# Kernel optimization log

Measured on AMD Instinct MI355X. Metric: run time of the kernel, lower is better.

## Reference

```python
import jax, jax.numpy as jnp
import numpy as np

B, N, D, K = 16, 512, 256, 12  # batch, nodes, node_dim, num edge types (4 arg + 4 arg' + punct +/- + no_edges +/-)
ITERATION_STEPS = 1


def setup_inputs() -> dict:
    key = jax.random.key(0)
    ks = jax.random.split(key, 8)
    node = jax.random.normal(ks[0], (B, N, D), dtype=jnp.float32)
    node_mask = jax.random.randint(ks[1], (B, N), 0, 2, dtype=jnp.int32)
    graphs = jax.random.randint(ks[2], (K, B, N, N), 0, 2, dtype=jnp.int32)
    s = 1.0 / np.sqrt(D)
    Ww = jax.random.normal(ks[3], (1, D), dtype=jnp.float32) * s   # _node_weight_fc
    bw = jnp.zeros((1,), dtype=jnp.float32)
    Ws = jax.random.normal(ks[4], (D, D), dtype=jnp.float32) * s   # _self_node_fc
    bs = jnp.zeros((D,), dtype=jnp.float32)
    Wk = jax.random.normal(ks[5], (K, D, D), dtype=jnp.float32) * s  # 12 bias-free per-edge-type linears
    return {"node": node, "Ww": Ww, "bw": bw, "Ws": Ws, "bs": bs, "Wk": Wk,
            "node_mask": node_mask, "graphs": graphs}


def reference(node, Ww, bw, Ws, bs, Wk, node_mask, graphs):
    dt = node.dtype
    mask = node_mask.astype(dt)
    eye = jnp.eye(N, dtype=dt)
    # dd_graph = mask_row * mask_col * (1 - diag)
    dd = mask[:, None, :] * mask[:, :, None] * (1.0 - eye)          # [B,N,N]
    g = dd[None] * graphs.astype(dt)                                # [K,B,N,N] masked adjacencies
    neigh = g.sum(axis=(0, 3))                                      # [B,N] total neighbor count
    neigh = jnp.where(neigh >= 1, neigh, jnp.ones((), dt))

    all_w = []
    for _ in range(ITERATION_STEPS):
        # (1) node relatedness
        w = jax.nn.sigmoid(node @ Ww.T + bw)[..., 0]                # [B,N]
        all_w.append(w)
        self_info = node @ Ws.T + bs                                # [B,N,D]
        # (2) message propagation for all 12 edge types, batched
        trans = jnp.einsum('bnd,ked->kbne', node, Wk)               # [K,B,N,D] per-type linear (x @ W.T)
        wg = w[None, :, None, :] * g                                # [K,B,N,N] masked node weights
        agg = jnp.einsum('kbmn,kbnd->bmd', wg, trans) / neigh[..., None]
        # (3) update
        node = jax.nn.relu(self_info + agg)

    all_weight = jnp.stack(all_w, axis=1)                           # [B,steps,N]
    return node, all_weight
```

## Files before the change

kernel.cpp:

```cpp
#include <hip/hip_runtime.h>
#include <hip/hip_bf16.h>
#include <math.h>

#define BB 16
#define NN 512
#define DD 256
#define KK 12

typedef __bf16 bf16x8 __attribute__((ext_vector_type(8)));
typedef __bf16 bf16x4 __attribute__((ext_vector_type(4)));
typedef float  f32x4  __attribute__((ext_vector_type(4)));

#define WS_WM     0
#define WS_NCNT   32768
#define WS_MASKBF 65536
#define WS_NODEBF 81920
#define WS_NODET  4276224
#define WS_WKBF   8470528
#define WS_WSBF   10043392
#define WS_AGG    10174464

__global__ __launch_bounds__(256) void k1_prep(const float* __restrict__ node,
        const float* __restrict__ Ww, const float* __restrict__ bw,
        const int* __restrict__ node_mask,
        float* __restrict__ wm, __bf16* __restrict__ maskbf,
        __bf16* __restrict__ node_bf, float* __restrict__ all_w) {
    int t = threadIdx.x;
    int lane = t & 63;
    int row = blockIdx.x * 4 + (t >> 6);
    const float4 nv = *(const float4*)(node + (size_t)row * DD + lane * 4);
    const float4 wv = *(const float4*)(Ww + lane * 4);
    float dot = nv.x*wv.x + nv.y*wv.y + nv.z*wv.z + nv.w*wv.w;
    #pragma unroll
    for (int off = 32; off > 0; off >>= 1) dot += __shfl_xor(dot, off);
    float w = 1.0f / (1.0f + expf(-(dot + bw[0])));
    int mk = node_mask[row];
    if (lane == 0) {
        wm[row]     = w * (float)mk;
        all_w[row]  = w;
        maskbf[row] = (__bf16)(float)mk;
    }
    bf16x4 nb = {(__bf16)nv.x, (__bf16)nv.y, (__bf16)nv.z, (__bf16)nv.w};
    *(bf16x4*)(node_bf + (size_t)row * DD + lane * 4) = nb;
}

__global__ __launch_bounds__(256) void k1b_convert(const float* __restrict__ Wk,
        const float* __restrict__ Ws, __bf16* __restrict__ Wk_bf, __bf16* __restrict__ Ws_bf) {
    const int KDD = KK * DD * DD;
    int idx = (blockIdx.x * 256 + threadIdx.x) * 4;
    if (idx < KDD) {
        float4 v = *(const float4*)(Wk + idx);
        bf16x4 o = {(__bf16)v.x, (__bf16)v.y, (__bf16)v.z, (__bf16)v.w};
        *(bf16x4*)(Wk_bf + idx) = o;
    } else {
        int j = idx - KDD;
        if (j < DD * DD) {
            float4 v = *(const float4*)(Ws + j);
            bf16x4 o = {(__bf16)v.x, (__bf16)v.y, (__bf16)v.z, (__bf16)v.w};
            *(bf16x4*)(Ws_bf + j) = o;
        }
    }
}

__global__ __launch_bounds__(256) void k2_transpose(const float* __restrict__ node,
        const float* __restrict__ wm, __bf16* __restrict__ dst) {
    __shared__ float tile[64][65];
    int bx = blockIdx.x;
    int b = bx >> 5; int rest = bx & 31; int nt = rest >> 2; int dt = rest & 3;
    int n0 = nt * 64, d0 = dt * 64;
    int t = threadIdx.x;
    #pragma unroll
    for (int i = 0; i < 16; i++) {
        int idx = i * 256 + t;
        int n = idx >> 6, d = idx & 63;
        tile[n][d] = node[((size_t)(b * NN + n0 + n)) * DD + d0 + d];
    }
    __syncthreads();
    #pragma unroll
    for (int i = 0; i < 16; i++) {
        int idx = i * 256 + t;
        int d = idx >> 6, n = idx & 63;
        float w = wm[b * NN + n0 + n];
        dst[((size_t)(b * DD + d0 + d)) * NN + n0 + n] = (__bf16)(tile[n][d] * w);
    }
}

__global__ __launch_bounds__(512, 2) void k45_partial(const int* __restrict__ graphs,
        const __bf16* __restrict__ maskbf, const __bf16* __restrict__ node_t,
        const __bf16* __restrict__ Wk_bf, float* __restrict__ Agg, int* __restrict__ ncnt) {
    __shared__ __align__(16) __bf16 Abf[32][520];
    __shared__ __align__(16) __bf16 Tk[32][264];
    __shared__ float cntp[8][32];
    int bx = blockIdx.x;
    int b  = (bx & 7) + 8 * ((bx >> 3) & 1);
    int kh = (bx >> 4) & 1;
    int mt = bx >> 5;
    int m0 = mt * 32;
    int t = threadIdx.x;
    int lane = t & 63;
    int w = t >> 6;
    int q = lane >> 4;
    int l16 = lane & 15;
    int esub = w * 32;
    int dsub = w * 32;

    int crow = t >> 7;
    int ccol = (t & 127) * 4;

    f32x4 accO[2][2];
    #pragma unroll
    for (int i = 0; i < 2; i++)
        #pragma unroll
        for (int j = 0; j < 2; j++) accO[i][j] = (f32x4){0.f, 0.f, 0.f, 0.f};
    f32x4 accC[2];
    accC[0] = (f32x4){0.f, 0.f, 0.f, 0.f};
    accC[1] = (f32x4){0.f, 0.f, 0.f, 0.f};

    int4 g[8];
    {
        const int4* gb = (const int4*)(graphs + ((size_t)((kh * 6 * BB + b) * NN + m0)) * NN);
        #pragma unroll
        for (int u = 0; u < 8; u++) g[u] = gb[u * 512 + t];
    }

    #pragma unroll 1
    for (int kc = 0; kc < 6; kc++) {
        int k = kh * 6 + kc;
        #pragma unroll
        for (int u = 0; u < 8; u++) {
            int row = u * 4 + crow;
            unsigned p0 = (unsigned)g[u].x | ((unsigned)g[u].y << 16);
            unsigned p1 = (unsigned)g[u].z | ((unsigned)g[u].w << 16);
            unsigned drel = (unsigned)(m0 + row - ccol);
            if (drel < 2u)      p0 &= ~(0xFFFFu << (16 * drel));
            else if (drel < 4u) p1 &= ~(0xFFFFu << (16 * (drel - 2)));
            uint2 st; st.x = p0 * 0x3F80u; st.y = p1 * 0x3F80u;
            *(uint2*)&Abf[row][ccol] = st;
        }
        __syncthreads();

        if (kc < 5) {
            const int4* gb = (const int4*)(graphs + ((size_t)(((k + 1) * BB + b) * NN + m0)) * NN);
            #pragma unroll
            for (int u = 0; u < 8; u++) g[u] = gb[u * 512 + t];
        }

        f32x4 accT[2][2];
        #pragma unroll
        for (int i = 0; i < 2; i++)
            #pragma unroll
            for (int j = 0; j < 2; j++) accT[i][j] = (f32x4){0.f, 0.f, 0.f, 0.f};
        #pragma unroll
        for (int kk = 0; kk < 16; kk++) {
            int n0c = kk * 32;
            bf16x8 af[2], bfr[2];
            #pragma unroll
            for (int fm = 0; fm < 2; fm++)
                af[fm] = *(const bf16x8*)&Abf[fm * 16 + l16][n0c + q * 8];
            #pragma unroll
            for (int fd = 0; fd < 2; fd++)
                bfr[fd] = *(const bf16x8*)(node_t +
                    ((size_t)(b * DD + esub + fd * 16 + l16)) * NN + n0c + q * 8);
            #pragma unroll
            for (int fm = 0; fm < 2; fm++)
                #pragma unroll
                for (int fd = 0; fd < 2; fd++)
                    accT[fm][fd] = __builtin_amdgcn_mfma_f32_16x16x32_bf16(
                        af[fm], bfr[fd], accT[fm][fd], 0, 0, 0);
            if ((kk >> 1) == w) {
                bf16x8 bfm = (bf16x8){0,0,0,0,0,0,0,0};
                if (l16 == 0)
                    bfm = *(const bf16x8*)(maskbf + b * NN + n0c + q * 8);
                accC[0] = __builtin_amdgcn_mfma_f32_16x16x32_bf16(af[0], bfm, accC[0], 0, 0, 0);
                accC[1] = __builtin_amdgcn_mfma_f32_16x16x32_bf16(af[1], bfm, accC[1], 0, 0, 0);
            }
        }
        #pragma unroll
        for (int fm = 0; fm < 2; fm++)
            #pragma unroll
            for (int fd = 0; fd < 2; fd++) {
                int col = esub + fd * 16 + l16;
                #pragma unroll
                for (int r = 0; r < 4; r++)
                    Tk[fm * 16 + q * 4 + r][col] = (__bf16)accT[fm][fd][r];
            }
        __syncthreads();

        #pragma unroll
        for (int ee = 0; ee < 8; ee++) {
            int e0c = ee * 32;
            bf16x8 afT[2], bw2[2];
            #pragma unroll
            for (int fm = 0; fm < 2; fm++)
                afT[fm] = *(const bf16x8*)&Tk[fm * 16 + l16][e0c + q * 8];
            #pragma unroll
            for (int fd = 0; fd < 2; fd++)
                bw2[fd] = *(const bf16x8*)(Wk_bf +
                    ((size_t)(k * DD + dsub + fd * 16 + l16)) * DD + e0c + q * 8);
            #pragma unroll
            for (int fm = 0; fm < 2; fm++)
                #pragma unroll
                for (int fd = 0; fd < 2; fd++)
                    accO[fm][fd] = __builtin_amdgcn_mfma_f32_16x16x32_bf16(
                        afT[fm], bw2[fd], accO[fm][fd], 0, 0, 0);
        }
    }

    if (l16 == 0) {
        #pragma unroll
        for (int fm = 0; fm < 2; fm++)
            #pragma unroll
            for (int r = 0; r < 4; r++)
                cntp[w][fm * 16 + q * 4 + r] = accC[fm][r];
    }
    __syncthreads();
    if (t < 32) {
        float c = 0.0f;
        #pragma unroll
        for (int w8 = 0; w8 < 8; w8++) c += cntp[w8][t];
        atomicAdd(&ncnt[b * NN + m0 + t], (int)(c + 0.5f));
    }

    float* Ah = Agg + (size_t)kh * BB * NN * DD;
    #pragma unroll
    for (int fm = 0; fm < 2; fm++)
        #pragma unroll
        for (int fd = 0; fd < 2; fd++) {
            int d = dsub + fd * 16 + l16;
            #pragma unroll
            for (int r = 0; r < 4; r++) {
                int m = m0 + fm * 16 + q * 4 + r;
                Ah[((size_t)(b * NN + m)) * DD + d] = accO[fm][fd][r];
            }
        }
}

__global__ __launch_bounds__(256) void k6_epilogue(const float* __restrict__ Agg,
        const __bf16* __restrict__ node_bf, const __bf16* __restrict__ Ws_bf,
        const float* __restrict__ bs, const int* __restrict__ ncnt,
        const int* __restrict__ node_mask, float* __restrict__ out) {
    __shared__ float sm[16];
    int bx = blockIdx.x;
    int b = bx & 15;
    int mt = bx >> 4;
    int m0 = mt * 16;
    int t = threadIdx.x;
    int lane = t & 63;
    int w = t >> 6;
    int q = lane >> 4;
    int l16 = lane & 15;
    int dsub = w * 64;

    if (t < 16) {
        int c = ncnt[b * NN + m0 + t];
        int mk = node_mask[b * NN + m0 + t];
        sm[t] = (float)mk / (float)(c >= 1 ? c : 1);
    }

    f32x4 accS[4];
    #pragma unroll
    for (int i = 0; i < 4; i++) accS[i] = (f32x4){0.f, 0.f, 0.f, 0.f};
    #pragma unroll
    for (int ee = 0; ee < 8; ee++) {
        int e0c = ee * 32;
        bf16x8 afS = *(const bf16x8*)(node_bf +
            ((size_t)(b * NN + m0 + l16)) * DD + e0c + q * 8);
        bf16x8 bwS[4];
        #pragma unroll
        for (int fd = 0; fd < 4; fd++)
            bwS[fd] = *(const bf16x8*)(Ws_bf +
                ((size_t)(dsub + fd * 16 + l16)) * DD + e0c + q * 8);
        #pragma unroll
        for (int fd = 0; fd < 4; fd++)
            accS[fd] = __builtin_amdgcn_mfma_f32_16x16x32_bf16(afS, bwS[fd], accS[fd], 0, 0, 0);
    }
    __syncthreads();

    const float* A0 = Agg;
    const float* A1 = Agg + (size_t)BB * NN * DD;
    #pragma unroll
    for (int fd = 0; fd < 4; fd++) {
        int d = dsub + fd * 16 + l16;
        float bsv = bs[d];
        #pragma unroll
        for (int r = 0; r < 4; r++) {
            int m = m0 + q * 4 + r;
            size_t idx = ((size_t)(b * NN + m)) * DD + d;
            float v = sm[q * 4 + r] * (A0[idx] + A1[idx]) + accS[fd][r] + bsv;
            out[idx] = fmaxf(v, 0.0f);
        }
    }
}

extern "C" void kernel_launch(void* const* d_in, const int* in_sizes, int n_in,
                              void* d_out, int out_size, void* d_ws, size_t ws_size,
                              hipStream_t stream) {
    const float* node      = (const float*)d_in[0];
    const float* Ww        = (const float*)d_in[1];
    const float* bw        = (const float*)d_in[2];
    const float* Ws        = (const float*)d_in[3];
    const float* bs        = (const float*)d_in[4];
    const float* Wk        = (const float*)d_in[5];
    const int*   node_mask = (const int*)d_in[6];
    const int*   graphs    = (const int*)d_in[7];
    float* out   = (float*)d_out;
    float* all_w = out + (size_t)BB * NN * DD;

    char* ws = (char*)d_ws;
    float*  wm      = (float*)(ws + WS_WM);
    int*    ncnt    = (int*)(ws + WS_NCNT);
    __bf16* maskbf  = (__bf16*)(ws + WS_MASKBF);
    __bf16* node_bf = (__bf16*)(ws + WS_NODEBF);
    __bf16* node_t  = (__bf16*)(ws + WS_NODET);
    __bf16* Wk_bf   = (__bf16*)(ws + WS_WKBF);
    __bf16* Ws_bf   = (__bf16*)(ws + WS_WSBF);
    float*  Agg     = (float*)(ws + WS_AGG);

    hipMemsetAsync(ncnt, 0, BB * NN * sizeof(int), stream);
    k1_prep    <<<2048, 256, 0, stream>>>(node, Ww, bw, node_mask, wm, maskbf, node_bf, all_w);
    k1b_convert<<< 832, 256, 0, stream>>>(Wk, Ws, Wk_bf, Ws_bf);
    k2_transpose<<<512, 256, 0, stream>>>(node, wm, node_t);
    k45_partial<<< 512, 512, 0, stream>>>(graphs, maskbf, node_t, Wk_bf, Agg, ncnt);
    k6_epilogue<<< 512, 256, 0, stream>>>(Agg, node_bf, Ws_bf, bs, ncnt, node_mask, out);
}
```

Measured before the change: 373.6 us.

## Split edge types four ways with smaller blocks and blob-layout partial aggregates

The main aggregation kernel now splits the 12 edge types into four groups of three instead of two groups of six. It launches 1024 blocks of 256 threads, and each wave covers 64 output columns instead of 32. Graph loads are no longer prefetched across iterations; they are loaded directly per half-tile. Partial aggregates are written as contiguous per-thread float4 blobs, and the epilogue reads and sums the four partials with vector loads over 32-row tiles. The aim is more parallelism and coalesced partial stores, at the cost of twice the partial-aggregate traffic and lost load/compute overlap.

```diff
diff --git a/kernel.cpp b/kernel.cpp
--- a/kernel.cpp
+++ b/kernel.cpp
@@ -19,6 +19,7 @@
 #define WS_WKBF   8470528
 #define WS_WSBF   10043392
 #define WS_AGG    10174464
+#define AGG_KQ_STRIDE 2097152
 
 __global__ __launch_bounds__(256) void k1_prep(const float* __restrict__ node,
         const float* __restrict__ Ww, const float* __restrict__ bw,
@@ -85,89 +86,83 @@
     }
 }
 
-__global__ __launch_bounds__(512, 2) void k45_partial(const int* __restrict__ graphs,
+__global__ __launch_bounds__(256) void k45_partial(const int* __restrict__ graphs,
         const __bf16* __restrict__ maskbf, const __bf16* __restrict__ node_t,
-        const __bf16* __restrict__ Wk_bf, float* __restrict__ Agg, int* __restrict__ ncnt) {
+        const __bf16* __restrict__ Wk_bf, float* __restrict__ AggBlob, int* __restrict__ ncnt) {
     __shared__ __align__(16) __bf16 Abf[32][520];
     __shared__ __align__(16) __bf16 Tk[32][264];
-    __shared__ float cntp[8][32];
+    __shared__ float cntp[4][32];
     int bx = blockIdx.x;
     int b  = (bx & 7) + 8 * ((bx >> 3) & 1);
-    int kh = (bx >> 4) & 1;
-    int mt = bx >> 5;
+    int kq = (bx >> 4) & 3;
+    int mt = bx >> 6;
     int m0 = mt * 32;
     int t = threadIdx.x;
     int lane = t & 63;
     int w = t >> 6;
     int q = lane >> 4;
     int l16 = lane & 15;
-    int esub = w * 32;
-    int dsub = w * 32;
-
-    int crow = t >> 7;
-    int ccol = (t & 127) * 4;
-
-    f32x4 accO[2][2];
+    int esub = w * 64;
+    int dsub = w * 64;
+
+    int rowpar = t >> 7;
+    int ccol   = (t & 127) * 4;
+
+    f32x4 accO[2][4];
     #pragma unroll
     for (int i = 0; i < 2; i++)
         #pragma unroll
-        for (int j = 0; j < 2; j++) accO[i][j] = (f32x4){0.f, 0.f, 0.f, 0.f};
+        for (int j = 0; j < 4; j++) accO[i][j] = (f32x4){0.f, 0.f, 0.f, 0.f};
     f32x4 accC[2];
     accC[0] = (f32x4){0.f, 0.f, 0.f, 0.f};
     accC[1] = (f32x4){0.f, 0.f, 0.f, 0.f};
 
-    int4 g[8];
-    {
-        const int4* gb = (const int4*)(graphs + ((size_t)((kh * 6 * BB + b) * NN + m0)) * NN);
-        #pragma unroll
-        for (int u = 0; u < 8; u++) g[u] = gb[u * 512 + t];
-    }
-
     #pragma unroll 1
-    for (int kc = 0; kc < 6; kc++) {
-        int k = kh * 6 + kc;
-        #pragma unroll
-        for (int u = 0; u < 8; u++) {
-            int row = u * 4 + crow;
-            unsigned p0 = (unsigned)g[u].x | ((unsigned)g[u].y << 16);
-            unsigned p1 = (unsigned)g[u].z | ((unsigned)g[u].w << 16);
-            unsigned drel = (unsigned)(m0 + row - ccol);
-            if (drel < 2u)      p0 &= ~(0xFFFFu << (16 * drel));
-            else if (drel < 4u) p1 &= ~(0xFFFFu << (16 * (drel - 2)));
-            uint2 st; st.x = p0 * 0x3F80u; st.y = p1 * 0x3F80u;
-            *(uint2*)&Abf[row][ccol] = st;
+    for (int kc = 0; kc < 3; kc++) {
+        int k = kq * 3 + kc;
+        #pragma unroll
+        for (int h = 0; h < 2; h++) {
+            const int4* gb = (const int4*)(graphs + ((size_t)((k * BB + b) * NN + m0 + h * 16)) * NN);
+            int4 g[8];
+            #pragma unroll
+            for (int u = 0; u < 8; u++) g[u] = gb[u * 256 + t];
+            #pragma unroll
+            for (int u = 0; u < 8; u++) {
+                int row = h * 16 + u * 2 + rowpar;
+                unsigned p0 = (unsigned)g[u].x | ((unsigned)g[u].y << 16);
+                unsigned p1 = (unsigned)g[u].z | ((unsigned)g[u].w << 16);
+                unsigned drel = (unsigned)(m0 + row - ccol);
+                if (drel < 2u)      p0 &= ~(0xFFFFu << (16 * drel));
+                else if (drel < 4u) p1 &= ~(0xFFFFu << (16 * (drel - 2)));
+                uint2 st; st.x = p0 * 0x3F80u; st.y = p1 * 0x3F80u;
+                *(uint2*)&Abf[row][ccol] = st;
+            }
         }
         __syncthreads();
 
-        if (kc < 5) {
-            const int4* gb = (const int4*)(graphs + ((size_t)(((k + 1) * BB + b) * NN + m0)) * NN);
-            #pragma unroll
-            for (int u = 0; u < 8; u++) g[u] = gb[u * 512 + t];
-        }
-
-        f32x4 accT[2][2];
+        f32x4 accT[2][4];
         #pragma unroll
         for (int i = 0; i < 2; i++)
             #pragma unroll
-            for (int j = 0; j < 2; j++) accT[i][j] = (f32x4){0.f, 0.f, 0.f, 0.f};
+            for (int j = 0; j < 4; j++) accT[i][j] = (f32x4){0.f, 0.f, 0.f, 0.f};
         #pragma unroll
         for (int kk = 0; kk < 16; kk++) {
             int n0c = kk * 32;
-            bf16x8 af[2], bfr[2];
+            bf16x8 af[2], bfr[4];
             #pragma unroll
             for (int fm = 0; fm < 2; fm++)
                 af[fm] = *(const bf16x8*)&Abf[fm * 16 + l16][n0c + q * 8];
             #pragma unroll
-            for (int fd = 0; fd < 2; fd++)
+            for (int fd = 0; fd < 4; fd++)
                 bfr[fd] = *(const bf16x8*)(node_t +
                     ((size_t)(b * DD + esub + fd * 16 + l16)) * NN + n0c + q * 8);
             #pragma unroll
             for (int fm = 0; fm < 2; fm++)
                 #pragma unroll
-                for (int fd = 0; fd < 2; fd++)
+                for (int fd = 0; fd < 4; fd++)
                     accT[fm][fd] = __builtin_amdgcn_mfma_f32_16x16x32_bf16(
                         af[fm], bfr[fd], accT[fm][fd], 0, 0, 0);
-            if ((kk >> 1) == w) {
+            if ((kk >> 2) == w) {
                 bf16x8 bfm = (bf16x8){0,0,0,0,0,0,0,0};
                 if (l16 == 0)
                     bfm = *(const bf16x8*)(maskbf + b * NN + n0c + q * 8);
@@ -178,7 +173,7 @@
         #pragma unroll
         for (int fm = 0; fm < 2; fm++)
             #pragma unroll
-            for (int fd = 0; fd < 2; fd++) {
+            for (int fd = 0; fd < 4; fd++) {
                 int col = esub + fd * 16 + l16;
                 #pragma unroll
                 for (int r = 0; r < 4; r++)
@@ -189,18 +184,18 @@
         #pragma unroll
         for (int ee = 0; ee < 8; ee++) {
             int e0c = ee * 32;
-            bf16x8 afT[2], bw2[2];
+            bf16x8 afT[2], bw2[4];
             #pragma unroll
             for (int fm = 0; fm < 2; fm++)
                 afT[fm] = *(const bf16x8*)&Tk[fm * 16 + l16][e0c + q * 8];
             #pragma unroll
-            for (int fd = 0; fd < 2; fd++)
+            for (int fd = 0; fd < 4; fd++)
                 bw2[fd] = *(const bf16x8*)(Wk_bf +
                     ((size_t)(k * DD + dsub + fd * 16 + l16)) * DD + e0c + q * 8);
             #pragma unroll
             for (int fm = 0; fm < 2; fm++)
                 #pragma unroll
-                for (int fd = 0; fd < 2; fd++)
+                for (int fd = 0; fd < 4; fd++)
                     accO[fm][fd] = __builtin_amdgcn_mfma_f32_16x16x32_bf16(
                         afT[fm], bw2[fd], accO[fm][fd], 0, 0, 0);
         }
@@ -215,35 +210,27 @@
     }
     __syncthreads();
     if (t < 32) {
-        float c = 0.0f;
-        #pragma unroll
-        for (int w8 = 0; w8 < 8; w8++) c += cntp[w8][t];
+        float c = cntp[0][t] + cntp[1][t] + cntp[2][t] + cntp[3][t];
         atomicAdd(&ncnt[b * NN + m0 + t], (int)(c + 0.5f));
     }
 
-    float* Ah = Agg + (size_t)kh * BB * NN * DD;
+    float* Ah = AggBlob + (size_t)kq * AGG_KQ_STRIDE + (((size_t)(b * 16 + mt)) * 256 + t) * 32;
     #pragma unroll
     for (int fm = 0; fm < 2; fm++)
         #pragma unroll
-        for (int fd = 0; fd < 2; fd++) {
-            int d = dsub + fd * 16 + l16;
-            #pragma unroll
-            for (int r = 0; r < 4; r++) {
-                int m = m0 + fm * 16 + q * 4 + r;
-                Ah[((size_t)(b * NN + m)) * DD + d] = accO[fm][fd][r];
-            }
-        }
-}
-
-__global__ __launch_bounds__(256) void k6_epilogue(const float* __restrict__ Agg,
+        for (int fd = 0; fd < 4; fd++)
+            *(f32x4*)(Ah + (fm * 4 + fd) * 4) = accO[fm][fd];
+}
+
+__global__ __launch_bounds__(256) void k6_epilogue(const float* __restrict__ AggBlob,
         const __bf16* __restrict__ node_bf, const __bf16* __restrict__ Ws_bf,
         const float* __restrict__ bs, const int* __restrict__ ncnt,
         const int* __restrict__ node_mask, float* __restrict__ out) {
-    __shared__ float sm[16];
+    __shared__ float sm[32];
     int bx = blockIdx.x;
-    int b = bx & 15;
+    int b  = (bx & 7) + 8 * ((bx >> 3) & 1);
     int mt = bx >> 4;
-    int m0 = mt * 16;
+    int m0 = mt * 32;
     int t = threadIdx.x;
     int lane = t & 63;
     int w = t >> 6;
@@ -251,45 +238,66 @@
     int l16 = lane & 15;
     int dsub = w * 64;
 
-    if (t < 16) {
-        int c = ncnt[b * NN + m0 + t];
+    if (t < 32) {
+        int c  = ncnt[b * NN + m0 + t];
         int mk = node_mask[b * NN + m0 + t];
         sm[t] = (float)mk / (float)(c >= 1 ? c : 1);
     }
 
-    f32x4 accS[4];
-    #pragma unroll
-    for (int i = 0; i < 4; i++) accS[i] = (f32x4){0.f, 0.f, 0.f, 0.f};
+    const float* base = AggBlob + (((size_t)(b * 16 + mt)) * 256 + t) * 32;
+    f32x4 agg[8];
+    #pragma unroll
+    for (int j = 0; j < 8; j++) agg[j] = *(const f32x4*)(base + j * 4);
+    #pragma unroll
+    for (int kq = 1; kq < 4; kq++) {
+        const float* bq = base + (size_t)kq * AGG_KQ_STRIDE;
+        #pragma unroll
+        for (int j = 0; j < 8; j++) {
+            f32x4 v = *(const f32x4*)(bq + j * 4);
+            agg[j] += v;
+        }
+    }
+
+    f32x4 accS[2][4];
+    #pragma unroll
+    for (int i = 0; i < 2; i++)
+        #pragma unroll
+        for (int j = 0; j < 4; j++) accS[i][j] = (f32x4){0.f, 0.f, 0.f, 0.f};
     #pragma unroll
     for (int ee = 0; ee < 8; ee++) {
         int e0c = ee * 32;
-        bf16x8 afS = *(const bf16x8*)(node_bf +
-            ((size_t)(b * NN + m0 + l16)) * DD + e0c + q * 8);
-        bf16x8 bwS[4];
+        bf16x8 afS[2], bwS[4];
+        #pragma unroll
+        for (int fm = 0; fm < 2; fm++)
+            afS[fm] = *(const bf16x8*)(node_bf +
+                ((size_t)(b * NN + m0 + fm * 16 + l16)) * DD + e0c + q * 8);
         #pragma unroll
         for (int fd = 0; fd < 4; fd++)
             bwS[fd] = *(const bf16x8*)(Ws_bf +
                 ((size_t)(dsub + fd * 16 + l16)) * DD + e0c + q * 8);
         #pragma unroll
-        for (int fd = 0; fd < 4; fd++)
-            accS[fd] = __builtin_amdgcn_mfma_f32_16x16x32_bf16(afS, bwS[fd], accS[fd], 0, 0, 0);
+        for (int fm = 0; fm < 2; fm++)
+            #pragma unroll
+            for (int fd = 0; fd < 4; fd++)
+                accS[fm][fd] = __builtin_amdgcn_mfma_f32_16x16x32_bf16(
+                    afS[fm], bwS[fd], accS[fm][fd], 0, 0, 0);
     }
     __syncthreads();
 
-    const float* A0 = Agg;
-    const float* A1 = Agg + (size_t)BB * NN * DD;
-    #pragma unroll
-    for (int fd = 0; fd < 4; fd++) {
-        int d = dsub + fd * 16 + l16;
-        float bsv = bs[d];
-        #pragma unroll
-        for (int r = 0; r < 4; r++) {
-            int m = m0 + q * 4 + r;
-            size_t idx = ((size_t)(b * NN + m)) * DD + d;
-            float v = sm[q * 4 + r] * (A0[idx] + A1[idx]) + accS[fd][r] + bsv;
-            out[idx] = fmaxf(v, 0.0f);
-        }
-    }
+    #pragma unroll
+    for (int fm = 0; fm < 2; fm++)
+        #pragma unroll
+        for (int fd = 0; fd < 4; fd++) {
+            int d = dsub + fd * 16 + l16;
+            float bsv = bs[d];
+            int j = fm * 4 + fd;
+            #pragma unroll
+            for (int r = 0; r < 4; r++) {
+                int m = m0 + fm * 16 + q * 4 + r;
+                float v = sm[fm * 16 + q * 4 + r] * agg[j][r] + accS[fm][fd][r] + bsv;
+                out[((size_t)(b * NN + m)) * DD + d] = fmaxf(v, 0.0f);
+            }
+        }
 }
 
 extern "C" void kernel_launch(void* const* d_in, const int* in_sizes, int n_in,
@@ -320,6 +328,6 @@
     k1_prep    <<<2048, 256, 0, stream>>>(node, Ww, bw, node_mask, wm, maskbf, node_bf, all_w);
     k1b_convert<<< 832, 256, 0, stream>>>(Wk, Ws, Wk_bf, Ws_bf);
     k2_transpose<<<512, 256, 0, stream>>>(node, wm, node_t);
-    k45_partial<<< 512, 512, 0, stream>>>(graphs, maskbf, node_t, Wk_bf, Agg, ncnt);
-    k6_epilogue<<< 512, 256, 0, stream>>>(Agg, node_bf, Ws_bf, bs, ncnt, node_mask, out);
-}
+    k45_partial<<<1024, 256, 0, stream>>>(graphs, maskbf, node_t, Wk_bf, Agg, ncnt);
+    k6_epilogue<<< 256, 256, 0, stream>>>(Agg, node_bf, Ws_bf, bs, ncnt, node_mask, out);
+}
```

After: 410.5 us. +9.9%, slower.
